# Kernel optimization log

Hardware: AMD Instinct MI355X
Metric: run time of the kernel (lower is better)

## Reference

```python
import jax, jax.numpy as jnp
import numpy as np

B, N = 64, 196
D1, D2, H = 512, 2048, 512


def setup_inputs() -> dict:
    key = jax.random.key(0)
    ks = jax.random.split(key, 8)
    s1 = 1.0 / np.sqrt(D1)
    s2 = 1.0 / np.sqrt(D2)
    sh = 1.0 / np.sqrt(H)
    return {
        "input1": jax.random.normal(ks[0], (B, D1), jnp.float32),
        "input2": jax.random.normal(ks[1], (B, N, D2), jnp.float32),
        "W1": jax.random.uniform(ks[2], (D1, H), jnp.float32, -s1, s1),
        "b1": jax.random.uniform(ks[3], (H,), jnp.float32, -s1, s1),
        "W2": jax.random.uniform(ks[4], (D2, H), jnp.float32, -s2, s2),
        "b2": jax.random.uniform(ks[5], (H,), jnp.float32, -s2, s2),
        "Wf": jax.random.uniform(ks[6], (H, 1), jnp.float32, -sh, sh),
        "bf": jax.random.uniform(ks[7], (1,), jnp.float32, -sh, sh),
    }


def reference(input1, input2, W1, b1, W2, b2, Wf, bf):
    # enc1: [B, H]; enc2: [B, N, H]
    enc1 = input1 @ W1 + b1
    enc2 = jnp.einsum("bnd,dh->bnh", input2, W2) + b2
    # additive (Bahdanau) score: relu(enc2 + enc1[:,None]) @ Wf -> [B, N]
    scores = (jax.nn.relu(enc2 + enc1[:, None, :]) @ Wf)[..., 0] + bf[0]
    alpha = jax.nn.softmax(scores, axis=1)  # softmax over N regions
    att = jnp.einsum("bnd,bn->bd", input2, alpha)  # weighted sum of raw features
    return att, alpha
```

## Files before the change

### kernel.cpp

```cpp
#include <hip/hip_runtime.h>
#include <hip/hip_bf16.h>
#include <stdint.h>

#define BB 64
#define NN 196
#define D1c 512
#define D2c 2048
#define HHc 512
#define MM (BB*NN)

typedef __attribute__((ext_vector_type(8))) short bf16x8;
typedef __attribute__((ext_vector_type(4))) float f32x4;

__device__ inline ushort f2bf(float f){
  uint32_t u = __float_as_uint(f);
  u += 0x7fff + ((u >> 16) & 1);
  return (ushort)(u >> 16);
}
__device__ inline uint32_t cvtpk(float lo, float hi){
  uint32_t r;
  asm("v_cvt_pk_bf16_f32 %0, %1, %2" : "=v"(r) : "v"(lo), "v"(hi));
  return r;
}

__global__ __launch_bounds__(256) void w2t_kernel(const float* __restrict__ W2,
                                                  ushort* __restrict__ w2t){
  __shared__ float tile[64][65];
  const int ktb = blockIdx.x;
  const int ht  = blockIdx.y;
  const int t = threadIdx.x;
  const int tr = t >> 4;
  const int tc = (t & 15) * 4;
  #pragma unroll
  for (int p = 0; p < 4; ++p){
    int k = p*16 + tr;
    float4 v = *(const float4*)(W2 + (size_t)(ktb*64 + k)*HHc + ht*64 + tc);
    tile[k][tc] = v.x; tile[k][tc+1] = v.y; tile[k][tc+2] = v.z; tile[k][tc+3] = v.w;
  }
  __syncthreads();
  #pragma unroll
  for (int pp = 0; pp < 4; ++pp){
    int hl = pp*16 + tr;
    ushort4 o;
    o.x = f2bf(tile[tc  ][hl]);
    o.y = f2bf(tile[tc+1][hl]);
    o.z = f2bf(tile[tc+2][hl]);
    o.w = f2bf(tile[tc+3][hl]);
    size_t addr = (size_t)(ht*4 + pp)*32768 + (size_t)ktb*1024
                + (size_t)((tc>>5)&1)*512 + (size_t)((tc>>3)&3)*128
                + (size_t)tr*8 + (tc & 4);
    *(ushort4*)(w2t + addr) = o;
  }
}

__global__ __launch_bounds__(128) void enc1_kernel(const float* __restrict__ in1,
                                                   const float* __restrict__ W1,
                                                   const float* __restrict__ b1,
                                                   float* __restrict__ enc1){
  __shared__ float s1[D1c];
  const int b = blockIdx.x;
  const int ht = blockIdx.y;
  const int t = threadIdx.x;
  ((float4*)s1)[t] = ((const float4*)(in1 + (size_t)b*D1c))[t];
  __syncthreads();
  const int h = ht*128 + t;
  float acc = b1[h];
  #pragma unroll 8
  for (int d = 0; d < D1c; ++d)
    acc += s1[d] * W1[(size_t)d*HHc + h];
  enc1[b*HHc + h] = acc;
}

__global__ __launch_bounds__(256,3) void score_gemm(
    const float*  __restrict__ in2,
    const ushort* __restrict__ w2t,
    const float*  __restrict__ b2,
    const float*  __restrict__ wf,
    const float*  __restrict__ enc1,
    float*        __restrict__ scores)
{
  __shared__ ushort As[2][64*64];

  const int t = threadIdx.x;
  const int p  = blockIdx.x;
  const int lg = (p & 7) * 98 + (p >> 3);
  const int h0 = (lg & 3) * 128;
  const int m0 = (lg >> 2) * 64;

  const int wave = t >> 6, lane = t & 63;
  const int l15 = lane & 15, l4 = lane >> 4;

  const int rA = wave*16 + l4;
  const float* aBase = in2 + (size_t)(m0 + rA)*D2c + l15*4;
  const int acw = l15 >> 1;
  const int apar = (l15 & 1) * 4;

  const ushort* bBase = w2t + (size_t)h0*2048 + (size_t)wave*65536 + lane*8;

  float b2v[2], wfv[2];
  #pragma unroll
  for (int hf = 0; hf < 2; ++hf){
    int hc = h0 + wave*32 + hf*16 + l15;
    b2v[hf] = b2[hc]; wfv[hf] = wf[hc];
  }

  f32x4 acc[4][2];
  #pragma unroll
  for (int i = 0; i < 4; ++i)
    #pragma unroll
    for (int j = 0; j < 2; ++j) acc[i][j] = (f32x4)0.f;

  float4 aRegA[4], aRegB[4];
  bf16x8 bRegA[4], bRegB[4];

#define A_LOAD(kt, R)                                                        \
  { _Pragma("unroll")                                                        \
    for (int j = 0; j < 4; ++j)                                              \
      R[j] = *(const float4*)(aBase + (size_t)(j*4)*D2c + (kt)*64); }

#define B_LOAD(kt, Bv)                                                       \
  { _Pragma("unroll")                                                        \
    for (int f = 0; f < 4; ++f)                                              \
      Bv[f] = *(const bf16x8*)(bBase + (f>>1)*32768 + (kt)*1024 + (f&1)*512); }

#define A_WRITE(R, buf)                                                      \
  { _Pragma("unroll")                                                        \
    for (int j = 0; j < 4; ++j){                                             \
      int r = rA + j*4;                                                      \
      uint2 pk;                                                              \
      pk.x = cvtpk(R[j].x, R[j].y);                                          \
      pk.y = cvtpk(R[j].z, R[j].w);                                          \
      *(uint2*)(As[buf] + r*64 + ((acw ^ (r & 7)) << 3) + apar) = pk; } }

#define COMPUTE(buf, Bv)                                                     \
  { _Pragma("unroll")                                                        \
    for (int kk = 0; kk < 2; ++kk){                                          \
      bf16x8 af[4];                                                          \
      _Pragma("unroll")                                                      \
      for (int mf = 0; mf < 4; ++mf){                                        \
        int r = mf*16 + l15, c = kk*4 + l4;                                  \
        af[mf] = *(const bf16x8*)(As[buf] + r*64 + ((c ^ (r & 7)) << 3)); }  \
      _Pragma("unroll")                                                      \
      for (int mf = 0; mf < 4; ++mf)                                         \
        _Pragma("unroll")                                                    \
        for (int hf = 0; hf < 2; ++hf)                                       \
          acc[mf][hf] = __builtin_amdgcn_mfma_f32_16x16x32_bf16(             \
              af[mf], Bv[hf*2+kk], acc[mf][hf], 0, 0, 0); } }

#define LGKM0() asm volatile("s_waitcnt lgkmcnt(0)" ::: "memory")
#define SB0()   __builtin_amdgcn_sched_barrier(0)
#define BAR()   { SB0(); __builtin_amdgcn_s_barrier(); SB0(); }

  A_LOAD(0, aRegA);
  B_LOAD(0, bRegA);
  A_LOAD(1, aRegB);
  A_WRITE(aRegA, 0);
  LGKM0();
  BAR();

  #pragma unroll 1
  for (int kt = 0; kt < 30; kt += 2){
    B_LOAD(kt + 1, bRegB);
    A_LOAD(kt + 2, aRegA);
    COMPUTE(0, bRegA);
    A_WRITE(aRegB, 1);
    LGKM0();
    BAR();
    B_LOAD(kt + 2, bRegA);
    A_LOAD(kt + 3, aRegB);
    COMPUTE(1, bRegB);
    A_WRITE(aRegA, 0);
    LGKM0();
    BAR();
  }
  B_LOAD(31, bRegB);
  COMPUTE(0, bRegA);
  A_WRITE(aRegB, 1);
  LGKM0();
  BAR();
  COMPUTE(1, bRegB);

  #pragma unroll
  for (int mf = 0; mf < 4; ++mf){
    #pragma unroll
    for (int r = 0; r < 4; ++r){
      int m = m0 + mf*16 + l4*4 + r;
      int b = m / NN;
      const float* e1 = enc1 + (size_t)b*HHc + h0 + wave*32 + l15;
      float s = 0.f;
      #pragma unroll
      for (int hf = 0; hf < 2; ++hf){
        float v = acc[mf][hf][r] + b2v[hf] + e1[hf*16];
        s += fmaxf(v, 0.f) * wfv[hf];
      }
      s += __shfl_xor(s, 1); s += __shfl_xor(s, 2);
      s += __shfl_xor(s, 4); s += __shfl_xor(s, 8);
      if (l15 == 0) atomicAdd(&scores[m], s);
    }
  }
#undef A_LOAD
#undef B_LOAD
#undef A_WRITE
#undef COMPUTE
#undef LGKM0
#undef SB0
#undef BAR
}

__global__ __launch_bounds__(64) void softmax_kernel(const float* __restrict__ scores,
                                                     float* __restrict__ alpha){
  const int b = blockIdx.x, t = threadIdx.x;
  const float* s = scores + b*NN;
  float x[4]; float mx = -1e30f;
  #pragma unroll
  for (int i = 0; i < 4; ++i){
    int n = t + i*64;
    x[i] = (n < NN) ? s[n] : -1e30f;
    mx = fmaxf(mx, x[i]);
  }
  #pragma unroll
  for (int o = 1; o < 64; o <<= 1) mx = fmaxf(mx, __shfl_xor(mx, o));
  float sum = 0.f;
  #pragma unroll
  for (int i = 0; i < 4; ++i){
    int n = t + i*64;
    float e = (n < NN) ? __expf(x[i] - mx) : 0.f;
    x[i] = e; sum += e;
  }
  #pragma unroll
  for (int o = 1; o < 64; o <<= 1) sum += __shfl_xor(sum, o);
  float inv = 1.f / sum;
  #pragma unroll
  for (int i = 0; i < 4; ++i){
    int n = t + i*64;
    if (n < NN) alpha[b*NN + n] = x[i] * inv;
  }
}

__global__ __launch_bounds__(256) void att_kernel(const float* __restrict__ in2,
                                                  const float* __restrict__ alpha,
                                                  float* __restrict__ att){
  __shared__ float sal[NN];
  const int b = blockIdx.y;
  const int t = threadIdx.x;
  if (t < NN) sal[t] = alpha[b*NN + t];
  __syncthreads();
  const int d = blockIdx.x*256 + t;
  const float* src = in2 + (size_t)b*NN*D2c + d;
  float acc = 0.f;
  #pragma unroll 7
  for (int n = 0; n < NN; ++n)
    acc += src[(size_t)n*D2c] * sal[n];
  att[(size_t)b*D2c + d] = acc;
}

extern "C" void kernel_launch(void* const* d_in, const int* in_sizes, int n_in,
                              void* d_out, int out_size, void* d_ws, size_t ws_size,
                              hipStream_t stream){
  (void)in_sizes; (void)n_in; (void)out_size; (void)ws_size;
  const float* input1 = (const float*)d_in[0];
  const float* input2 = (const float*)d_in[1];
  const float* W1     = (const float*)d_in[2];
  const float* b1     = (const float*)d_in[3];
  const float* W2     = (const float*)d_in[4];
  const float* b2     = (const float*)d_in[5];
  const float* Wf     = (const float*)d_in[6];

  float* out   = (float*)d_out;
  float* att   = out;
  float* alpha = out + BB*D2c;

  char*   ws     = (char*)d_ws;
  ushort* w2t    = (ushort*)ws;
  float*  enc1   = (float*)(ws + 2*1024*1024);
  float*  scores = (float*)(ws + 2*1024*1024 + 131072);

  hipMemsetAsync(scores, 0, MM*sizeof(float), stream);
  w2t_kernel<<<dim3(32, 8), 256, 0, stream>>>(W2, w2t);
  enc1_kernel<<<dim3(BB, 4), 128, 0, stream>>>(input1, W1, b1, enc1);
  score_gemm<<<dim3(784), 256, 0, stream>>>(input2, w2t, b2, Wf, enc1, scores);
  softmax_kernel<<<dim3(BB), 64, 0, stream>>>(scores, alpha);
  att_kernel<<<dim3(8, BB), 256, 0, stream>>>(input2, alpha, att);
}
```

Before: 104.3 us.

## Deepen A-operand global prefetch to three stages in enc2 GEMM main loop

The K-loop now keeps four register sets for the fp32 A tiles and issues global loads three K-steps ahead instead of one. The loop is unrolled by four to rotate through these buffers, while B stays double-buffered in registers and A stays double-buffered in LDS. The aim is to hide more HBM latency on the streamed input2 reads. It costs extra VGPRs (48 more floats per lane), which may reduce occupancy or cause spills.

```diff
diff --git a/kernel.cpp b/kernel.cpp
--- a/kernel.cpp
+++ b/kernel.cpp
@@ -110,8 +110,8 @@
     #pragma unroll
     for (int j = 0; j < 2; ++j) acc[i][j] = (f32x4)0.f;
 
-  float4 aRegA[4], aRegB[4];
-  bf16x8 bRegA[4], bRegB[4];
+  float4 aS0[4], aS1[4], aS2[4], aS3[4];
+  bf16x8 b0[4], b1[4];
 
 #define A_LOAD(kt, R)                                                        \
   { _Pragma("unroll")                                                        \
@@ -151,34 +151,39 @@
 #define SB0()   __builtin_amdgcn_sched_barrier(0)
 #define BAR()   { SB0(); __builtin_amdgcn_s_barrier(); SB0(); }
 
-  A_LOAD(0, aRegA);
-  B_LOAD(0, bRegA);
-  A_LOAD(1, aRegB);
-  A_WRITE(aRegA, 0);
+  A_LOAD(0, aS0);
+  A_LOAD(1, aS1);
+  A_LOAD(2, aS2);
+  B_LOAD(0, b0);
+  A_WRITE(aS0, 0);
   LGKM0();
   BAR();
 
   #pragma unroll 1
-  for (int kt = 0; kt < 30; kt += 2){
-    B_LOAD(kt + 1, bRegB);
-    A_LOAD(kt + 2, aRegA);
-    COMPUTE(0, bRegA);
-    A_WRITE(aRegB, 1);
-    LGKM0();
-    BAR();
-    B_LOAD(kt + 2, bRegA);
-    A_LOAD(kt + 3, aRegB);
-    COMPUTE(1, bRegB);
-    A_WRITE(aRegA, 0);
-    LGKM0();
-    BAR();
-  }
-  B_LOAD(31, bRegB);
-  COMPUTE(0, bRegA);
-  A_WRITE(aRegB, 1);
-  LGKM0();
-  BAR();
-  COMPUTE(1, bRegB);
+  for (int kt = 0; kt < 28; kt += 4){
+    A_LOAD(kt + 3, aS3);  B_LOAD(kt + 1, b1);
+    COMPUTE(0, b0);
+    A_WRITE(aS1, 1);  LGKM0();  BAR();
+    A_LOAD(kt + 4, aS0);  B_LOAD(kt + 2, b0);
+    COMPUTE(1, b1);
+    A_WRITE(aS2, 0);  LGKM0();  BAR();
+    A_LOAD(kt + 5, aS1);  B_LOAD(kt + 3, b1);
+    COMPUTE(0, b0);
+    A_WRITE(aS3, 1);  LGKM0();  BAR();
+    A_LOAD(kt + 6, aS2);  B_LOAD(kt + 4, b0);
+    COMPUTE(1, b1);
+    A_WRITE(aS0, 0);  LGKM0();  BAR();
+  }
+  A_LOAD(31, aS3);  B_LOAD(29, b1);
+  COMPUTE(0, b0);
+  A_WRITE(aS1, 1);  LGKM0();  BAR();
+  B_LOAD(30, b0);
+  COMPUTE(1, b1);
+  A_WRITE(aS2, 0);  LGKM0();  BAR();
+  B_LOAD(31, b1);
+  COMPUTE(0, b0);
+  A_WRITE(aS3, 1);  LGKM0();  BAR();
+  COMPUTE(1, b1);
 
   #pragma unroll
   for (int mf = 0; mf < 4; ++mf){
```

After: 110.7 us. 1.06x slower.
